# Kernel tuning notes

Measured on AMD Instinct MI355X. Metric: run time of the kernel, lower is better.

## Reference

```python
import jax, jax.numpy as jnp
import numpy as np

N = 384       # nodes
K = 60        # neighbors per node
SUB = 20      # subsample_k
C_S = 128
C_Z = 128
H = 4
D_HEAD = C_Z // H
NUM_RBF = 64
E = N * K
EPS = 1e-8


def _rbf(D, D_min=0.0, D_max=20.0, D_count=NUM_RBF):
    # radial basis expansion of distances: [..., ] -> [..., D_count]
    mu = jnp.linspace(D_min, D_max, D_count)
    sigma = (D_max - D_min) / D_count
    return jnp.exp(-(((D[..., None] - mu) / sigma) ** 2))


def setup_inputs() -> dict:
    key = jax.random.key(0)
    ks = jax.random.split(key, 16)
    f32 = jnp.float32
    inp = {
        "node_features": jax.random.normal(ks[0], (N, C_S), f32),
        "node_trans": jax.random.normal(ks[1], (N, 3), f32) * 5.0,
        "edge_features": jax.random.normal(ks[2], (E, C_Z), f32),
        "edge_index": jax.random.randint(ks[3], (2, E), 0, N),
        "subsample_idx": jax.random.randint(ks[4], (N, K, SUB), 0, K),
        # dist_bias_gate: Linear(2*c_s -> H)
        "W_gate": jax.random.normal(ks[5], (2 * C_S, H), f32) / np.sqrt(2 * C_S),
        "b_gate": jnp.zeros((H,), f32),
        # dist_bias: Linear(num_rbf -> H)
        "W_db": jax.random.normal(ks[6], (NUM_RBF, H), f32) / np.sqrt(NUM_RBF),
        "b_db": jnp.zeros((H,), f32),
        # lin_qk: Linear(c_z -> 2*c_z)
        "W_qk": jax.random.normal(ks[7], (C_Z, 2 * C_Z), f32) / np.sqrt(C_Z),
        "b_qk": jnp.zeros((2 * C_Z,), f32),
        # lin_v: Linear(c_z -> c_z)
        "W_v": jax.random.normal(ks[8], (C_Z, C_Z), f32) / np.sqrt(C_Z),
        "b_v": jnp.zeros((C_Z,), f32),
        # lin_out: Linear(c_z -> c_z) (init='final' in source; random here for testing)
        "W_out": jax.random.normal(ks[9], (C_Z, C_Z), f32) / np.sqrt(C_Z),
        "b_out": jnp.zeros((C_Z,), f32),
    }
    return inp


def reference(node_features, node_trans, edge_features, edge_index, subsample_idx,
              W_gate, b_gate, W_db, b_db, W_qk, b_qk, W_v, b_v, W_out, b_out):
    n, k, sub = subsample_idx.shape
    # assume_sorted=True path: edges are grouped k-per-destination-node
    dst = edge_index[0].reshape(n, k)                           # [n,k] neighbor ids
    edge1 = jnp.broadcast_to(dst[:, :, None], (n, k, sub))      # [n,k,sub]
    edge2 = jnp.take_along_axis(
        jnp.broadcast_to(dst[:, None, :], (n, k, k)), subsample_idx, axis=-1)  # [n,k,sub]

    f1 = node_features[edge1]                                   # [n,k,sub,c_s]
    f2 = node_features[edge2]
    gate = jax.nn.sigmoid(jnp.concatenate([f1, f2], axis=-1) @ W_gate + b_gate)  # [n,k,sub,H]

    t1 = node_trans[edge1]                                      # [n,k,sub,3]
    t2 = node_trans[edge2]
    dist = jnp.linalg.norm(t1 - t2 + EPS, axis=-1)              # [n,k,sub]
    bias = gate * (_rbf(dist) @ W_db + b_db)                    # [n,k,sub,H]

    edges = edge_features.reshape(n, k, C_Z)
    qk = edges @ W_qk + b_qk
    q, kk = jnp.split(qk, 2, axis=-1)
    q = q.reshape(n, k, H, D_HEAD)
    kk = kk.reshape(n, k, H, D_HEAD)

    batch = jnp.arange(n)[:, None, None]
    k_sub = kk[batch, subsample_idx]                            # [n,k,sub,H,d]
    attn = jnp.einsum('nkhd,nkshd->nksh', q, k_sub) / np.sqrt(C_Z) + bias
    attn = jax.nn.softmax(attn, axis=2)                         # softmax over subsample axis

    v = (edges @ W_v + b_v).reshape(n, k, H, D_HEAD)
    v_sub = v[batch, subsample_idx]                             # [n,k,sub,H,d]
    upd = jnp.einsum('nksh,nkshd->nkhd', attn, v_sub).reshape(n * k, C_Z)
    return upd @ W_out + b_out                                  # [E, c_z]
```

## Files before the change

### kernel.cpp

```cpp
#include <hip/hip_runtime.h>
#include <hip/hip_bf16.h>

typedef unsigned short ushortT;
typedef __attribute__((ext_vector_type(8))) short bf16x8;
typedef __attribute__((ext_vector_type(4))) float f32x4;

#define N_NODES 384
#define KNBR 60
#define SUBK 20
#define NEDGE (N_NODES * KNBR)
#define EPSC 1e-8f
#define INV_SQRT_CZ 0.08838834764831845f
#define MU_STEP (20.0f / 63.0f)
#define INV_MU_STEP (63.0f / 20.0f)
#define INV_SIGMA 3.2f

__device__ __forceinline__ float bflo(unsigned int u) { return __uint_as_float(u << 16); }
__device__ __forceinline__ float bfhi(unsigned int u) { return __uint_as_float(u & 0xffff0000u); }
__device__ __forceinline__ ushortT f2bu(float v) {
  union { float f; unsigned int u; } c;
  c.f = v;
  return (ushortT)((c.u + 0x7fffu + ((c.u >> 16) & 1u)) >> 16);
}
__device__ __forceinline__ unsigned int pack2bf(float x, float y) {
  return (unsigned int)f2bu(x) | ((unsigned int)f2bu(y) << 16);
}
__device__ __forceinline__ ushortT f2h(float x) {
  _Float16 h = (_Float16)x;
  return __builtin_bit_cast(ushortT, h);
}
__device__ __forceinline__ float h2f(ushortT u) {
  return (float)__builtin_bit_cast(_Float16, u);
}

__global__ __launch_bounds__(256) void prep_kernel(
    const float* __restrict__ nf, const float* __restrict__ Wg, float* __restrict__ g,
    const float* __restrict__ Wqk, const float* __restrict__ bqk,
    const float* __restrict__ Wv, const float* __restrict__ bv,
    const float* __restrict__ Wout,
    ushortT* __restrict__ Wp1, ushortT* __restrict__ Wp2, float* __restrict__ bc) {
  int b = blockIdx.x, tid = threadIdx.x;
  if (b < 96) {
    int n = b * 4 + (tid >> 6), t = tid & 63;
    float a = nf[n * 128 + t];
    float bb = nf[n * 128 + 64 + t];
    float acc[8];
#pragma unroll
    for (int h = 0; h < 4; ++h) {
      acc[h]     = a * Wg[t * 4 + h]         + bb * Wg[(t + 64) * 4 + h];
      acc[4 + h] = a * Wg[(128 + t) * 4 + h] + bb * Wg[(192 + t) * 4 + h];
    }
#pragma unroll
    for (int i = 0; i < 8; ++i)
#pragma unroll
      for (int off = 32; off >= 1; off >>= 1) acc[i] += __shfl_xor(acc[i], off, 64);
    if (t == 0) {
#pragma unroll
      for (int i = 0; i < 8; ++i) g[n * 8 + i] = acc[i];
    }
  } else {
    int i = (b - 96) * 256 + tid;
    if (i < 49152) {
      int j = i & 7, l = (i >> 3) & 63, t = (i >> 9) & 3;
      int nt = (i >> 11) % 12, ny = (i >> 11) / 12;
      int nn = ny * 192 + nt * 16 + (l & 15);
      int k = t * 32 + (l >> 4) * 8 + j;
      float v = (nn < 256) ? Wqk[k * 256 + nn] : Wv[k * 128 + (nn - 256)];
      Wp1[i] = f2bu(v);
    } else {
      int i2 = i - 49152;
      int j = i2 & 7, l = (i2 >> 3) & 63, t = (i2 >> 9) & 3, nt = (i2 >> 11);
      int nn = nt * 16 + (l & 15);
      int k = t * 32 + (l >> 4) * 8 + j;
      Wp2[i2] = f2bu(Wout[k * 128 + nn]);
    }
    if (i < 384) bc[i] = (i < 256) ? bqk[i] : bv[i - 256];
  }
}

__global__ __launch_bounds__(512, 4) void fused_kernel(
    const float* __restrict__ ef, const ushortT* __restrict__ Wp1,
    const ushortT* __restrict__ Wp2, const float* __restrict__ bc,
    const float* __restrict__ bout, const float* __restrict__ g,
    const float* __restrict__ node_trans, const int* __restrict__ edge_index,
    const int* __restrict__ sub_idx, const float* __restrict__ W_db,
    const float* __restrict__ b_db, const float* __restrict__ b_gate,
    float* __restrict__ outp) {
  __shared__ __align__(16) ushortT kvb[KNBR * 256];
  __shared__ __align__(16) ushortT updq[64 * 136];
  __shared__ __align__(16) ushortT biasb[KNBR * SUBK * 4];
  __shared__ ushortT sub_lds[KNBR * SUBK];
  __shared__ float trs[KNBR * 3];
  __shared__ float gg[KNBR * 8];

  int n = blockIdx.x, tid = threadIdx.x;
  int e0 = n * KNBR;
  int w = tid >> 6, l = tid & 63;
  int lr = l & 15, lc = l >> 4;
  int rowA = (w & 3) * 16 + lr;
  int rowAc = min(rowA, KNBR - 1);

  if (tid < KNBR) {
    int dst = edge_index[e0 + tid];
#pragma unroll
    for (int c = 0; c < 3; ++c) trs[tid * 3 + c] = node_trans[dst * 3 + c];
#pragma unroll
    for (int i = 0; i < 8; ++i) gg[tid * 8 + i] = g[dst * 8 + i];
  }
  bf16x8 afrag[4];
#pragma unroll
  for (int t = 0; t < 4; ++t) {
    const float* ap = ef + (size_t)(e0 + rowAc) * 128 + t * 32 + lc * 8;
    float4 lo = *(const float4*)ap;
    float4 hi = *(const float4*)(ap + 4);
    bf16x8 a;
    a[0] = (short)f2bu(lo.x); a[1] = (short)f2bu(lo.y);
    a[2] = (short)f2bu(lo.z); a[3] = (short)f2bu(lo.w);
    a[4] = (short)f2bu(hi.x); a[5] = (short)f2bu(hi.y);
    a[6] = (short)f2bu(hi.z); a[7] = (short)f2bu(hi.w);
    afrag[t] = a;
  }

  int Tbase = (tid >> 8) * 12;
#pragma unroll
  for (int Ti = 0; Ti < 12; ++Ti) {
    int T = Tbase + Ti;
    f32x4 acc = {0.f, 0.f, 0.f, 0.f};
#pragma unroll
    for (int t = 0; t < 4; ++t) {
      bf16x8 bfrag = *(const bf16x8*)(Wp1 + ((T * 4 + t) * 64 + l) * 8);
      acc = __builtin_amdgcn_mfma_f32_16x16x32_bf16(bfrag, afrag[t], acc, 0, 0, 0);
    }
    int col0 = T * 16 + lc * 4;
    float4 bi = *(const float4*)(bc + col0);
    float o0 = acc[0] + bi.x, o1 = acc[1] + bi.y;
    float o2 = acc[2] + bi.z, o3 = acc[3] + bi.w;
    if (T < 8) {
      uint2 o;
      o.x = pack2bf(o0 * INV_SQRT_CZ, o1 * INV_SQRT_CZ);
      o.y = pack2bf(o2 * INV_SQRT_CZ, o3 * INV_SQRT_CZ);
      *(uint2*)(updq + rowA * 136 + col0) = o;
    } else if (rowA < KNBR) {
      uint2 o;
      o.x = pack2bf(o0, o1);
      o.y = pack2bf(o2, o3);
      int colk = col0 - 128;
      int base_b = (colk & 128) << 1;
      int d = colk & 127;
      int inner = ((d >> 3) & 1) * 128 + (((d >> 4) * 16) ^ ((rowA & 7) << 4)) + (d & 7) * 2;
      *(uint2*)((char*)kvb + rowA * 512 + base_b + inner) = o;
    }
  }
  __syncthreads();

  float4 bgv = *(const float4*)b_gate;
  float4 bdbv = *(const float4*)b_db;
  for (int p = tid; p < KNBR * SUBK; p += 512) {
    int kl = p / SUBK, s = p - kl * SUBK;
    int j = sub_idx[(size_t)(e0 + kl) * SUBK + s];
    sub_lds[p] = (ushortT)j;
    float dx = trs[kl * 3 + 0] - trs[j * 3 + 0] + EPSC;
    float dy = trs[kl * 3 + 1] - trs[j * 3 + 1] + EPSC;
    float dz = trs[kl * 3 + 2] - trs[j * 3 + 2] + EPSC;
    float dist = sqrtf(dx * dx + dy * dy + dz * dz);
    int r0 = (int)(dist * INV_MU_STEP + 0.5f);
    int rlo = max(r0 - 4, 0), rhi = min(r0 + 4, 63);
    float a0 = 0.f, a1 = 0.f, a2 = 0.f, a3 = 0.f;
    for (int r = rlo; r <= rhi; ++r) {
      float t = (dist - r * MU_STEP) * INV_SIGMA;
      float e = __expf(-t * t);
      float4 wv = ((const float4*)W_db)[r];
      a0 += e * wv.x; a1 += e * wv.y; a2 += e * wv.z; a3 += e * wv.w;
    }
    float g1 = gg[kl * 8 + 0] + gg[j * 8 + 4 + 0] + bgv.x;
    float g2 = gg[kl * 8 + 1] + gg[j * 8 + 4 + 1] + bgv.y;
    float g3 = gg[kl * 8 + 2] + gg[j * 8 + 4 + 2] + bgv.z;
    float g4 = gg[kl * 8 + 3] + gg[j * 8 + 4 + 3] + bgv.w;
    biasb[p * 4 + 0] = f2h((a0 + bdbv.x) / (1.0f + __expf(-g1)));
    biasb[p * 4 + 1] = f2h((a1 + bdbv.y) / (1.0f + __expf(-g2)));
    biasb[p * 4 + 2] = f2h((a2 + bdbv.z) / (1.0f + __expf(-g3)));
    biasb[p * 4 + 3] = f2h((a3 + bdbv.w) / (1.0f + __expf(-g4)));
  }
  __syncthreads();

  int row3 = tid >> 3, h = (tid >> 1) & 3, dh = tid & 1;
  int row3c = min(row3, KNBR - 1);
  int hdo = (h * 2 + dh) * 16;
  const char* kvbase = (const char*)kvb;
  float q0, q1, q2, q3, q4, q5, q6, q7, q8, q9, q10, q11, q12, q13, q14, q15;
  {
    const ushortT* qp = updq + row3 * 136 + h * 32 + dh * 16;
    uint4 u0 = *(const uint4*)qp;
    uint4 u1 = *(const uint4*)(qp + 8);
    q0 = bflo(u0.x); q1 = bfhi(u0.x); q2 = bflo(u0.y); q3 = bfhi(u0.y);
    q4 = bflo(u0.z); q5 = bfhi(u0.z); q6 = bflo(u0.w); q7 = bfhi(u0.w);
    q8 = bflo(u1.x); q9 = bfhi(u1.x); q10 = bflo(u1.y); q11 = bfhi(u1.y);
    q12 = bflo(u1.z); q13 = bfhi(u1.z); q14 = bflo(u1.w); q15 = bfhi(u1.w);
  }
  float den = 0.f;
  float v0 = 0.f, v1 = 0.f, v2 = 0.f, v3 = 0.f, v4 = 0.f, v5 = 0.f, v6 = 0.f, v7 = 0.f;
  float v8 = 0.f, v9 = 0.f, v10 = 0.f, v11 = 0.f, v12 = 0.f, v13 = 0.f, v14 = 0.f, v15 = 0.f;
#pragma unroll 4
  for (int s = 0; s < SUBK; ++s) {
    int j = sub_lds[row3c * SUBK + s];
    int off = hdo ^ ((j & 7) << 4);
    const char* kr = kvbase + j * 512;
    uint4 k0 = *(const uint4*)(kr + off);
    uint4 k1 = *(const uint4*)(kr + 128 + off);
    float dot = q0 * bflo(k0.x) + q1 * bfhi(k0.x) + q2 * bflo(k0.y) + q3 * bfhi(k0.y) +
                q4 * bflo(k0.z) + q5 * bfhi(k0.z) + q6 * bflo(k0.w) + q7 * bfhi(k0.w) +
                q8 * bflo(k1.x) + q9 * bfhi(k1.x) + q10 * bflo(k1.y) + q11 * bfhi(k1.y) +
                q12 * bflo(k1.z) + q13 * bfhi(k1.z) + q14 * bflo(k1.w) + q15 * bfhi(k1.w);
    dot += __shfl_xor(dot, 1);
    float p = __expf(dot + h2f(biasb[(row3c * SUBK + s) * 4 + h]));
    den += p;
    uint4 w0 = *(const uint4*)(kr + 256 + off);
    uint4 w1 = *(const uint4*)(kr + 384 + off);
    v0 += p * bflo(w0.x); v1 += p * bfhi(w0.x); v2 += p * bflo(w0.y); v3 += p * bfhi(w0.y);
    v4 += p * bflo(w0.z); v5 += p * bfhi(w0.z); v6 += p * bflo(w0.w); v7 += p * bfhi(w0.w);
    v8 += p * bflo(w1.x); v9 += p * bfhi(w1.x); v10 += p * bflo(w1.y); v11 += p * bfhi(w1.y);
    v12 += p * bflo(w1.z); v13 += p * bfhi(w1.z); v14 += p * bflo(w1.w); v15 += p * bfhi(w1.w);
  }
  float inv = 1.0f / den;
  {
    uint4 o;
    o.x = pack2bf(v0 * inv, v1 * inv);
    o.y = pack2bf(v2 * inv, v3 * inv);
    o.z = pack2bf(v4 * inv, v5 * inv);
    o.w = pack2bf(v6 * inv, v7 * inv);
    *(uint4*)(updq + row3 * 136 + h * 32 + dh * 16) = o;
    uint4 o2;
    o2.x = pack2bf(v8 * inv, v9 * inv);
    o2.y = pack2bf(v10 * inv, v11 * inv);
    o2.z = pack2bf(v12 * inv, v13 * inv);
    o2.w = pack2bf(v14 * inv, v15 * inv);
    *(uint4*)(updq + row3 * 136 + h * 32 + dh * 16 + 8) = o2;
  }
  __syncthreads();

  bf16x8 af2[4];
#pragma unroll
  for (int t = 0; t < 4; ++t)
    af2[t] = *(const bf16x8*)(updq + rowA * 136 + t * 32 + lc * 8);
  int T4base = (tid >> 8) * 4;
#pragma unroll
  for (int Ti = 0; Ti < 4; ++Ti) {
    int T = T4base + Ti;
    f32x4 acc = {0.f, 0.f, 0.f, 0.f};
#pragma unroll
    for (int t = 0; t < 4; ++t) {
      bf16x8 bfrag = *(const bf16x8*)(Wp2 + ((T * 4 + t) * 64 + l) * 8);
      acc = __builtin_amdgcn_mfma_f32_16x16x32_bf16(bfrag, af2[t], acc, 0, 0, 0);
    }
    if (rowA < KNBR) {
      int col0 = T * 16 + lc * 4;
      float4 bi = *(const float4*)(bout + col0);
      float4 o;
      o.x = acc[0] + bi.x; o.y = acc[1] + bi.y;
      o.z = acc[2] + bi.z; o.w = acc[3] + bi.w;
      *(float4*)(outp + (size_t)(e0 + rowA) * 128 + col0) = o;
    }
  }
}

extern "C" void kernel_launch(void* const* d_in, const int* in_sizes, int n_in, void* d_out,
                              int out_size, void* d_ws, size_t ws_size, hipStream_t stream) {
  const float* nf  = (const float*)d_in[0];
  const float* nt  = (const float*)d_in[1];
  const float* ef  = (const float*)d_in[2];
  const int*   ei  = (const int*)d_in[3];
  const int*   si  = (const int*)d_in[4];
  const float* Wg  = (const float*)d_in[5];
  const float* bg  = (const float*)d_in[6];
  const float* Wdb = (const float*)d_in[7];
  const float* bdb = (const float*)d_in[8];
  const float* Wqk = (const float*)d_in[9];
  const float* bqk = (const float*)d_in[10];
  const float* Wv  = (const float*)d_in[11];
  const float* bv  = (const float*)d_in[12];
  const float* Wout = (const float*)d_in[13];
  const float* bout = (const float*)d_in[14];
  float* out = (float*)d_out;

  float* g      = (float*)d_ws;
  float* bc     = g + 3072;
  ushortT* Wp1  = (ushortT*)(bc + 384);
  ushortT* Wp2  = Wp1 + 49152;

  prep_kernel<<<dim3(352), dim3(256), 0, stream>>>(nf, Wg, g, Wqk, bqk, Wv, bv, Wout,
                                                   Wp1, Wp2, bc);
  fused_kernel<<<dim3(N_NODES), dim3(512), 0, stream>>>(ef, Wp1, Wp2, bc, bout, g, nt, ei, si,
                                                        Wdb, bdb, bg, out);
}
```

Before: 40.69 us.

## Warp-specialize QKV projection and distance-bias computation to run concurrently

Splits the block so waves 0-3 compute 20 of the 24 QKV MFMA tiles while waves 4-7 compute the RBF/gate bias and then the remaining 4 tiles, removing one barrier between the two phases. The node-translation and gate gathers are spread over two waves, and a barrier is added before the projection. The 1/sqrt(c_z) query scale is folded into the prepacked weights and bias so it is no longer applied per element. The work split between the two wave groups may be uneven, which can leave waves idle at the next barrier, and the larger unrolled tile loop raises register pressure.

```diff
diff --git a/kernel.cpp b/kernel.cpp
--- a/kernel.cpp
+++ b/kernel.cpp
@@ -66,6 +66,7 @@
       int nn = ny * 192 + nt * 16 + (l & 15);
       int k = t * 32 + (l >> 4) * 8 + j;
       float v = (nn < 256) ? Wqk[k * 256 + nn] : Wv[k * 128 + (nn - 256)];
+      if (nn < 128) v *= INV_SQRT_CZ;
       Wp1[i] = f2bu(v);
     } else {
       int i2 = i - 49152;
@@ -74,7 +75,11 @@
       int k = t * 32 + (l >> 4) * 8 + j;
       Wp2[i2] = f2bu(Wout[k * 128 + nn]);
     }
-    if (i < 384) bc[i] = (i < 256) ? bqk[i] : bv[i - 256];
+    if (i < 384) {
+      float v = (i < 256) ? bqk[i] : bv[i - 256];
+      if (i < 128) v *= INV_SQRT_CZ;
+      bc[i] = v;
+    }
   }
 }
 
@@ -100,13 +105,18 @@
   int rowA = (w & 3) * 16 + lr;
   int rowAc = min(rowA, KNBR - 1);
 
-  if (tid < KNBR) {
-    int dst = edge_index[e0 + tid];
-#pragma unroll
-    for (int c = 0; c < 3; ++c) trs[tid * 3 + c] = node_trans[dst * 3 + c];
-#pragma unroll
-    for (int i = 0; i < 8; ++i) gg[tid * 8 + i] = g[dst * 8 + i];
-  }
+  if (w == 4 && l < KNBR) {
+    int dst = edge_index[e0 + l];
+#pragma unroll
+    for (int c = 0; c < 3; ++c) trs[l * 3 + c] = node_trans[dst * 3 + c];
+  }
+  if (w == 5 && l < KNBR) {
+    int dst = edge_index[e0 + l];
+#pragma unroll
+    for (int i = 0; i < 8; ++i) gg[l * 8 + i] = g[dst * 8 + i];
+  }
+  __syncthreads();
+
   bf16x8 afrag[4];
 #pragma unroll
   for (int t = 0; t < 4; ++t) {
@@ -121,65 +131,69 @@
     afrag[t] = a;
   }
 
-  int Tbase = (tid >> 8) * 12;
-#pragma unroll
-  for (int Ti = 0; Ti < 12; ++Ti) {
-    int T = Tbase + Ti;
-    f32x4 acc = {0.f, 0.f, 0.f, 0.f};
-#pragma unroll
-    for (int t = 0; t < 4; ++t) {
-      bf16x8 bfrag = *(const bf16x8*)(Wp1 + ((T * 4 + t) * 64 + l) * 8);
-      acc = __builtin_amdgcn_mfma_f32_16x16x32_bf16(bfrag, afrag[t], acc, 0, 0, 0);
-    }
-    int col0 = T * 16 + lc * 4;
-    float4 bi = *(const float4*)(bc + col0);
-    float o0 = acc[0] + bi.x, o1 = acc[1] + bi.y;
-    float o2 = acc[2] + bi.z, o3 = acc[3] + bi.w;
-    if (T < 8) {
-      uint2 o;
-      o.x = pack2bf(o0 * INV_SQRT_CZ, o1 * INV_SQRT_CZ);
-      o.y = pack2bf(o2 * INV_SQRT_CZ, o3 * INV_SQRT_CZ);
-      *(uint2*)(updq + rowA * 136 + col0) = o;
-    } else if (rowA < KNBR) {
-      uint2 o;
-      o.x = pack2bf(o0, o1);
-      o.y = pack2bf(o2, o3);
-      int colk = col0 - 128;
-      int base_b = (colk & 128) << 1;
-      int d = colk & 127;
-      int inner = ((d >> 3) & 1) * 128 + (((d >> 4) * 16) ^ ((rowA & 7) << 4)) + (d & 7) * 2;
-      *(uint2*)((char*)kvb + rowA * 512 + base_b + inner) = o;
-    }
-  }
-  __syncthreads();
-
-  float4 bgv = *(const float4*)b_gate;
-  float4 bdbv = *(const float4*)b_db;
-  for (int p = tid; p < KNBR * SUBK; p += 512) {
-    int kl = p / SUBK, s = p - kl * SUBK;
-    int j = sub_idx[(size_t)(e0 + kl) * SUBK + s];
-    sub_lds[p] = (ushortT)j;
-    float dx = trs[kl * 3 + 0] - trs[j * 3 + 0] + EPSC;
-    float dy = trs[kl * 3 + 1] - trs[j * 3 + 1] + EPSC;
-    float dz = trs[kl * 3 + 2] - trs[j * 3 + 2] + EPSC;
-    float dist = sqrtf(dx * dx + dy * dy + dz * dz);
-    int r0 = (int)(dist * INV_MU_STEP + 0.5f);
-    int rlo = max(r0 - 4, 0), rhi = min(r0 + 4, 63);
-    float a0 = 0.f, a1 = 0.f, a2 = 0.f, a3 = 0.f;
-    for (int r = rlo; r <= rhi; ++r) {
-      float t = (dist - r * MU_STEP) * INV_SIGMA;
-      float e = __expf(-t * t);
-      float4 wv = ((const float4*)W_db)[r];
-      a0 += e * wv.x; a1 += e * wv.y; a2 += e * wv.z; a3 += e * wv.w;
-    }
-    float g1 = gg[kl * 8 + 0] + gg[j * 8 + 4 + 0] + bgv.x;
-    float g2 = gg[kl * 8 + 1] + gg[j * 8 + 4 + 1] + bgv.y;
-    float g3 = gg[kl * 8 + 2] + gg[j * 8 + 4 + 2] + bgv.z;
-    float g4 = gg[kl * 8 + 3] + gg[j * 8 + 4 + 3] + bgv.w;
-    biasb[p * 4 + 0] = f2h((a0 + bdbv.x) / (1.0f + __expf(-g1)));
-    biasb[p * 4 + 1] = f2h((a1 + bdbv.y) / (1.0f + __expf(-g2)));
-    biasb[p * 4 + 2] = f2h((a2 + bdbv.z) / (1.0f + __expf(-g3)));
-    biasb[p * 4 + 3] = f2h((a3 + bdbv.w) / (1.0f + __expf(-g4)));
+#define TILE_BODY(T)                                                                   \
+  {                                                                                    \
+    f32x4 acc = {0.f, 0.f, 0.f, 0.f};                                                  \
+    _Pragma("unroll") for (int t = 0; t < 4; ++t) {                                    \
+      bf16x8 bfrag = *(const bf16x8*)(Wp1 + (((T) * 4 + t) * 64 + l) * 8);             \
+      acc = __builtin_amdgcn_mfma_f32_16x16x32_bf16(bfrag, afrag[t], acc, 0, 0, 0);    \
+    }                                                                                  \
+    int col0 = (T) * 16 + lc * 4;                                                      \
+    float4 bi = *(const float4*)(bc + col0);                                           \
+    float o0 = acc[0] + bi.x, o1 = acc[1] + bi.y;                                      \
+    float o2 = acc[2] + bi.z, o3 = acc[3] + bi.w;                                      \
+    if ((T) < 8) {                                                                     \
+      uint2 o;                                                                         \
+      o.x = pack2bf(o0, o1);                                                           \
+      o.y = pack2bf(o2, o3);                                                           \
+      *(uint2*)(updq + rowA * 136 + col0) = o;                                         \
+    } else if (rowA < KNBR) {                                                          \
+      uint2 o;                                                                         \
+      o.x = pack2bf(o0, o1);                                                           \
+      o.y = pack2bf(o2, o3);                                                           \
+      int colk = col0 - 128;                                                           \
+      int base_b = (colk & 128) << 1;                                                  \
+      int d = colk & 127;                                                              \
+      int inner = ((d >> 3) & 1) * 128 + (((d >> 4) * 16) ^ ((rowA & 7) << 4)) +       \
+                  (d & 7) * 2;                                                         \
+      *(uint2*)((char*)kvb + rowA * 512 + base_b + inner) = o;                         \
+    }                                                                                  \
+  }
+
+  if (w < 4) {
+#pragma unroll
+    for (int T = 0; T < 20; ++T) TILE_BODY(T)
+  } else {
+    float4 bgv = *(const float4*)b_gate;
+    float4 bdbv = *(const float4*)b_db;
+    for (int p = tid - 256; p < KNBR * SUBK; p += 256) {
+      int kl = p / SUBK, s = p - kl * SUBK;
+      int j = sub_idx[(size_t)(e0 + kl) * SUBK + s];
+      sub_lds[p] = (ushortT)j;
+      float dx = trs[kl * 3 + 0] - trs[j * 3 + 0] + EPSC;
+      float dy = trs[kl * 3 + 1] - trs[j * 3 + 1] + EPSC;
+      float dz = trs[kl * 3 + 2] - trs[j * 3 + 2] + EPSC;
+      float dist = sqrtf(dx * dx + dy * dy + dz * dz);
+      int r0 = (int)(dist * INV_MU_STEP + 0.5f);
+      int rlo = max(r0 - 4, 0), rhi = min(r0 + 4, 63);
+      float a0 = 0.f, a1 = 0.f, a2 = 0.f, a3 = 0.f;
+      for (int r = rlo; r <= rhi; ++r) {
+        float t = (dist - r * MU_STEP) * INV_SIGMA;
+        float e = __expf(-t * t);
+        float4 wv = ((const float4*)W_db)[r];
+        a0 += e * wv.x; a1 += e * wv.y; a2 += e * wv.z; a3 += e * wv.w;
+      }
+      float g1 = gg[kl * 8 + 0] + gg[j * 8 + 4 + 0] + bgv.x;
+      float g2 = gg[kl * 8 + 1] + gg[j * 8 + 4 + 1] + bgv.y;
+      float g3 = gg[kl * 8 + 2] + gg[j * 8 + 4 + 2] + bgv.z;
+      float g4 = gg[kl * 8 + 3] + gg[j * 8 + 4 + 3] + bgv.w;
+      biasb[p * 4 + 0] = f2h((a0 + bdbv.x) / (1.0f + __expf(-g1)));
+      biasb[p * 4 + 1] = f2h((a1 + bdbv.y) / (1.0f + __expf(-g2)));
+      biasb[p * 4 + 2] = f2h((a2 + bdbv.z) / (1.0f + __expf(-g3)));
+      biasb[p * 4 + 3] = f2h((a3 + bdbv.w) / (1.0f + __expf(-g4)));
+    }
+#pragma unroll
+    for (int T = 20; T < 24; ++T) TILE_BODY(T)
   }
   __syncthreads();
 
@@ -261,6 +275,7 @@
       *(float4*)(outp + (size_t)(e0 + rowA) * 128 + col0) = o;
     }
   }
+#undef TILE_BODY
 }
 
 extern "C" void kernel_launch(void* const* d_in, const int* in_sizes, int n_in, void* d_out,
```

Measured after the change: 41.87 us. 1.03x slower.
